# Kernel tuning notes

Measured on AMD Instinct MI355X. Metric: run time of the kernel, lower is better.

Reference implementation:

```python
import jax, jax.numpy as jnp
import numpy as np

H = 8        # attention heads
G = 8        # groupnorm groups
EPS = 1e-5

def mish(x):
    return x * jnp.tanh(jnp.logaddexp(x, 0.0))

def conv1d(x, w, b, pad):
    # x: [B,C,L], w: [O,I,K]
    y = jax.lax.conv_general_dilated(x, w, (1,), [(pad, pad)],
                                     dimension_numbers=('NCH', 'OIH', 'NCH'))
    return y + b[None, :, None]

def gn_per_step(x, gamma, beta):
    # torch code reshapes [B,C,L] -> [(B L), C] and applies GroupNorm(G, C):
    # normalize each (b, l) position over channel groups.
    B, C, L = x.shape
    xg = x.reshape(B, G, C // G, L)
    mean = xg.mean(axis=2, keepdims=True)
    var = xg.var(axis=2, keepdims=True)
    xg = (xg - mean) * jax.lax.rsqrt(var + EPS)
    return xg.reshape(B, C, L) * gamma[None, :, None] + beta[None, :, None]

def layernorm(x, g, b):
    mean = x.mean(axis=-1, keepdims=True)
    var = x.var(axis=-1, keepdims=True)
    return (x - mean) * jax.lax.rsqrt(var + EPS) * g + b


def setup_inputs() -> dict:
    key = jax.random.key(0)
    ks = jax.random.split(key, 16)
    B, Cin, Cout, L, N, CD, TD = 64, 256, 512, 512, 77, 768, 512
    w = lambda k, shape, s=0.02: (jax.random.normal(k, shape, jnp.float32) * s)
    return {
        'x': jax.random.normal(ks[0], (B, Cin, L), jnp.float32),
        't': jax.random.normal(ks[1], (B, TD), jnp.float32),
        'cond': jax.random.normal(ks[2], (B, N, CD), jnp.float32),
        'conv0_w': w(ks[3], (Cout, Cin, 5)), 'conv0_b': jnp.zeros((Cout,), jnp.float32),
        'gn0_g': jnp.ones((Cout,), jnp.float32), 'gn0_b': jnp.zeros((Cout,), jnp.float32),
        'tm_w': w(ks[4], (2 * Cout, TD)), 'tm_b': jnp.zeros((2 * Cout,), jnp.float32),
        'conv1_w': w(ks[5], (Cout, Cout, 5)), 'conv1_b': jnp.zeros((Cout,), jnp.float32),
        'gn1_g': jnp.ones((Cout,), jnp.float32), 'gn1_b': jnp.zeros((Cout,), jnp.float32),
        'res_w': w(ks[6], (Cout, Cin, 1)), 'res_b': jnp.zeros((Cout,), jnp.float32),
        'ln_x_g': jnp.ones((Cout,), jnp.float32), 'ln_x_b': jnp.zeros((Cout,), jnp.float32),
        'ln_c_g': jnp.ones((CD,), jnp.float32), 'ln_c_b': jnp.zeros((CD,), jnp.float32),
        'q_w': w(ks[7], (Cout, Cout)), 'q_b': jnp.zeros((Cout,), jnp.float32),
        'k_w': w(ks[8], (Cout, CD)), 'k_b': jnp.zeros((Cout,), jnp.float32),
        'v_w': w(ks[9], (Cout, CD)), 'v_b': jnp.zeros((Cout,), jnp.float32),
        'cond_indices': jnp.arange(B, dtype=jnp.int64 if jax.config.jax_enable_x64 else jnp.int32),
    }


def _forward(x, t, cond,
             conv0_w, conv0_b, gn0_g, gn0_b, tm_w, tm_b,
             conv1_w, conv1_b, gn1_g, gn1_b, res_w, res_b,
             ln_x_g, ln_x_b, ln_c_g, ln_c_b,
             q_w, q_b, k_w, k_b, v_w, v_b, cond_indices):
    Cout = conv0_w.shape[0]
    # ---- ResidualTemporalBlock (adagn=True) ----
    ss = jnp.einsum('bi,oi->bo', mish(t), tm_w) + tm_b        # [B, 2*Cout]
    scale = ss[:, :Cout, None]                                 # chunk dim=1
    shift = ss[:, Cout:, None]
    h = conv1d(x, conv0_w, conv0_b, pad=2)                     # [B,Cout,L]
    h = gn_per_step(h, gn0_g, gn0_b)
    h = mish(h * (1.0 + scale) + shift)                        # ada_shift_scale + Mish
    h = conv1d(h, conv1_w, conv1_b, pad=2)
    h = mish(gn_per_step(h, gn1_g, gn1_b))
    out = h + conv1d(x, res_w, res_b, pad=0)                   # residual 1x1 conv
    # ---- ResidualCrossAttentionLayer (LinearCrossAttention) ----
    xs = out[cond_indices]                                     # [Bc,Cout,L]
    xi = xs.transpose(0, 2, 1)                                 # [Bc,L,Cout]
    cs = cond[cond_indices]                                    # [Bc,N,CD]
    Bc, T, D = xi.shape
    Nn = cs.shape[1]
    Dh = D // H
    q = jnp.einsum('btl,dl->btd', layernorm(xi, ln_x_g, ln_x_b), q_w) + q_b
    cn = layernorm(cs, ln_c_g, ln_c_b)
    k = jnp.einsum('bnl,dl->bnd', cn, k_w) + k_b
    v = jnp.einsum('bnl,dl->bnd', cn, v_w) + v_b
    q = jax.nn.softmax(q.reshape(Bc, T, H, Dh), axis=-1)       # softmax over head dim
    k = jax.nn.softmax(k.reshape(Bc, Nn, H, Dh), axis=1)       # softmax over tokens
    v = v.reshape(Bc, Nn, H, Dh)
    attn = jnp.einsum('bnhd,bnhl->bhdl', k, v)                 # [Bc,H,Dh,Dh] kernel
    y = jnp.einsum('bthd,bhdl->bthl', q, attn).reshape(Bc, T, D)
    return out.at[cond_indices].add(y.transpose(0, 2, 1))


def reference(x, t, cond,
              conv0_w, conv0_b, gn0_g, gn0_b, tm_w, tm_b,
              conv1_w, conv1_b, gn1_g, gn1_b, res_w, res_b,
              ln_x_g, ln_x_b, ln_c_g, ln_c_b,
              q_w, q_b, k_w, k_b, v_w, v_b, cond_indices):
    return _forward(x, t, cond, conv0_w, conv0_b, gn0_g, gn0_b, tm_w, tm_b,
                    conv1_w, conv1_b, gn1_g, gn1_b, res_w, res_b,
                    ln_x_g, ln_x_b, ln_c_g, ln_c_b,
                    q_w, q_b, k_w, k_b, v_w, v_b, cond_indices)
```

## Files before the change

### kernel.cpp

```cpp
#include <hip/hip_runtime.h>
#include <math.h>

#define EPS 1e-5f

typedef __attribute__((ext_vector_type(8))) short short8;
typedef __attribute__((ext_vector_type(4))) float floatx4;

typedef __attribute__((address_space(1))) const void* gas1_t;
typedef __attribute__((address_space(3))) void* las3_t;

__device__ __forceinline__ void glls16(const void* g, void* l) {
    __builtin_amdgcn_global_load_lds((gas1_t)g, (las3_t)l, 16, 0, 0);
}

__device__ __forceinline__ float mishf(float x) {
    float sp = fmaxf(x, 0.0f) + log1pf(expf(-fabsf(x)));
    return x * tanhf(sp);
}
__device__ __forceinline__ unsigned short f2bf(float f) {
    unsigned int u = __float_as_uint(f);
    unsigned int r = (u + 0x7fffu + ((u >> 16) & 1u)) >> 16;
    return (unsigned short)r;
}
__device__ __forceinline__ float bf2f(unsigned short s) {
    return __uint_as_float(((unsigned int)s) << 16);
}
__device__ __forceinline__ unsigned int pk2(unsigned short a, unsigned short b) {
    return (unsigned int)a | ((unsigned int)b << 16);
}

__global__ __launch_bounds__(256) void mish_k(const float* __restrict__ t,
                                              float* __restrict__ mt, int n) {
    int i = blockIdx.x * 256 + threadIdx.x;
    if (i < n) mt[i] = mishf(t[i]);
}

__global__ __launch_bounds__(256) void pack_w(const float* __restrict__ w,
        unsigned short* __restrict__ wp, int CI, int KS, int n) {
    int o = blockIdx.x * 256 + threadIdx.x;
    if (o >= n) return;
    int ci = o % CI;
    int co = (o / CI) & 511;
    int kk = o / (CI * 512);
    wp[o] = f2bf(w[((size_t)co * CI + ci) * KS + kk]);
}

__global__ __launch_bounds__(256) void cvt_bf16(const float* __restrict__ src,
        unsigned short* __restrict__ dst, int n4) {
    int i = blockIdx.x * 256 + threadIdx.x;
    if (i >= n4) return;
    float4 f = *(const float4*)&src[(size_t)i * 4];
    *(uint2*)&dst[(size_t)i * 4] =
        make_uint2(pk2(f2bf(f.x), f2bf(f.y)), pk2(f2bf(f.z), f2bf(f.w)));
}

__global__ __launch_bounds__(256) void xpose_cvt(const float* __restrict__ x,
        unsigned short* __restrict__ xT) {
    __shared__ float tile[64][68];
    const int tid = threadIdx.x;
    const int l0 = blockIdx.x * 64, c0 = blockIdx.y * 64, b = blockIdx.z;
    for (int idx = tid; idx < 64 * 16; idx += 256) {
        int cr = idx >> 4, lc = (idx & 15) * 4;
        float4 f = *(const float4*)&x[((size_t)b * 256 + c0 + cr) * 512 + l0 + lc];
        tile[cr][lc] = f.x; tile[cr][lc + 1] = f.y;
        tile[cr][lc + 2] = f.z; tile[cr][lc + 3] = f.w;
    }
    __syncthreads();
    for (int idx = tid; idx < 64 * 16; idx += 256) {
        int lr = idx >> 4, cc = (idx & 15) * 4;
        *(uint2*)&xT[((size_t)b * 512 + l0 + lr) * 256 + c0 + cc] =
            make_uint2(pk2(f2bf(tile[cc][lr]), f2bf(tile[cc + 1][lr])),
                       pk2(f2bf(tile[cc + 2][lr]), f2bf(tile[cc + 3][lr])));
    }
}

template<int KD>
__global__ __launch_bounds__(256) void gemm_nt(const float* __restrict__ A,
        const float* __restrict__ W, const float* __restrict__ bias,
        float* __restrict__ C, int M, int N) {
    constexpr int ST = 20;
    __shared__ __align__(16) float As[64 * ST];
    __shared__ __align__(16) float Ws[64 * ST];
    const int tid = threadIdx.x;
    const int r0 = blockIdx.x * 64, c0 = blockIdx.y * 64;
    const int tx = tid & 15, ty = tid >> 4;
    const int lrow = tid >> 2, lk = (tid & 3) * 4;
    float acc[4][4];
#pragma unroll
    for (int i = 0; i < 4; ++i)
#pragma unroll
        for (int j = 0; j < 4; ++j) acc[i][j] = 0.f;
    for (int k0 = 0; k0 < KD; k0 += 16) {
        __syncthreads();
        *(float4*)&As[lrow * ST + lk] =
            *(const float4*)&A[(size_t)(r0 + lrow) * KD + k0 + lk];
        *(float4*)&Ws[lrow * ST + lk] =
            *(const float4*)&W[(size_t)(c0 + lrow) * KD + k0 + lk];
        __syncthreads();
#pragma unroll
        for (int kk = 0; kk < 16; kk += 4) {
            float4 av[4], wv[4];
#pragma unroll
            for (int i = 0; i < 4; ++i)
                av[i] = *(const float4*)&As[(ty + 16 * i) * ST + kk];
#pragma unroll
            for (int j = 0; j < 4; ++j)
                wv[j] = *(const float4*)&Ws[(tx + 16 * j) * ST + kk];
#pragma unroll
            for (int i = 0; i < 4; ++i)
#pragma unroll
                for (int j = 0; j < 4; ++j) {
                    acc[i][j] = fmaf(av[i].x, wv[j].x, acc[i][j]);
                    acc[i][j] = fmaf(av[i].y, wv[j].y, acc[i][j]);
                    acc[i][j] = fmaf(av[i].z, wv[j].z, acc[i][j]);
                    acc[i][j] = fmaf(av[i].w, wv[j].w, acc[i][j]);
                }
        }
    }
#pragma unroll
    for (int j = 0; j < 4; ++j) {
        int c = c0 + tx + 16 * j;
        float bv = bias[c];
#pragma unroll
        for (int i = 0; i < 4; ++i)
            C[(size_t)(r0 + ty + 16 * i) * N + c] = acc[i][j] + bv;
    }
}

template<int CI, bool FILM>
__global__ __launch_bounds__(256) void conv5_mfma(
        const unsigned short* __restrict__ xb,
        const unsigned short* __restrict__ wp,
        const float* __restrict__ bias,
        const float* __restrict__ gam, const float* __restrict__ bet,
        const float* __restrict__ ss,
        unsigned short* __restrict__ outT) {
    __shared__ __align__(16) unsigned short xs[260 * 32];
    __shared__ __align__(16) unsigned short wsm[5 * 64 * 32];
    __shared__ float sgam[64], sbet[64], sbias[64], sscale[64], sshift[64];

    const int tid = threadIdx.x;
    const int l0 = blockIdx.x * 256;
    const int co0 = blockIdx.y * 64;
    const int b = blockIdx.z;
    const int lane = tid & 63;
    const int wv = tid >> 6;
    const int lq = lane & 15, qd = lane >> 4;
    const int wn = wv * 64;

    if (tid < 64) {
        int co = co0 + tid;
        sbias[tid] = bias[co];
        sgam[tid] = gam[co];
        sbet[tid] = bet[co];
        if (FILM) {
            sscale[tid] = ss[(size_t)b * 1024 + co];
            sshift[tid] = ss[(size_t)b * 1024 + 512 + co];
        }
    }

    floatx4 acc[4][4];
#pragma unroll
    for (int i = 0; i < 4; ++i)
#pragma unroll
        for (int j = 0; j < 4; ++j) acc[i][j] = (floatx4){0.f, 0.f, 0.f, 0.f};

    for (int ci0 = 0; ci0 < CI; ci0 += 32) {
        __syncthreads();
        if (tid < 128) {
            int rh = tid >> 5;
            int lr = (rh < 2) ? rh : (256 + rh);
            int ci_l = tid & 31;
            int gl = l0 - 2 + lr;
            unsigned short v = 0;
            if (gl >= 0 && gl < 512)
                v = xb[((size_t)b * 512 + gl) * CI + ci0 + ci_l];
            int pos = (ci_l >> 3) ^ ((lr >> 1) & 3);
            xs[lr * 32 + pos * 8 + (ci_l & 7)] = v;
        }
        {
            const unsigned short* gb = &xb[((size_t)b * 512 + l0) * CI + ci0];
#pragma unroll
            for (int it = 0; it < 4; ++it) {
                int task = it * 256 + wv * 64 + lane;
                int ri = task >> 2, pos = task & 3;
                int seg = pos ^ (((ri + 2) >> 1) & 3);
                glls16(gb + (size_t)ri * CI + seg * 8,
                       (void*)(xs + 64 + (it * 256 + wv * 64) * 8));
            }
        }
        {
#pragma unroll
            for (int it = 0; it < 5; ++it) {
                int task = it * 256 + wv * 64 + lane;
                int kk = task >> 8;
                int r = task & 255;
                int co_l = r >> 2, pos = r & 3;
                int seg = pos ^ ((co_l >> 1) & 3);
                glls16(&wp[((size_t)(kk * 512 + co0 + co_l)) * CI + ci0 + seg * 8],
                       (void*)(wsm + (it * 256 + wv * 64) * 8));
            }
        }
        __syncthreads();
#pragma unroll
        for (int kk = 0; kk < 5; ++kk) {
            short8 bvf[4];
#pragma unroll
            for (int j = 0; j < 4; ++j) {
                int row = wn + j * 16 + lq + kk;
                int pos = qd ^ ((row >> 1) & 3);
                bvf[j] = *(const short8*)&xs[row * 32 + pos * 8];
            }
#pragma unroll
            for (int i = 0; i < 4; ++i) {
                int crow = i * 16 + lq;
                int pos = qd ^ ((crow >> 1) & 3);
                short8 av = *(const short8*)&wsm[kk * 2048 + crow * 32 + pos * 8];
#pragma unroll
                for (int j = 0; j < 4; ++j)
                    acc[i][j] = __builtin_amdgcn_mfma_f32_16x16x32_bf16(
                        av, bvf[j], acc[i][j], 0, 0, 0);
            }
        }
    }
    float m_[4], rs_[4];
#pragma unroll
    for (int j = 0; j < 4; ++j) {
        float s1 = 0.f, s2 = 0.f;
#pragma unroll
        for (int i = 0; i < 4; ++i) {
            float4 bv4 = *(const float4*)&sbias[i * 16 + qd * 4];
            float ba[4] = {bv4.x, bv4.y, bv4.z, bv4.w};
#pragma unroll
            for (int r = 0; r < 4; ++r) {
                float v = acc[i][j][r] + ba[r];
                acc[i][j][r] = v;
                s1 += v; s2 += v * v;
            }
        }
        s1 += __shfl_xor(s1, 16, 64); s2 += __shfl_xor(s2, 16, 64);
        s1 += __shfl_xor(s1, 32, 64); s2 += __shfl_xor(s2, 32, 64);
        float mean = s1 * (1.f / 64.f);
        float var = s2 * (1.f / 64.f) - mean * mean;
        m_[j] = mean; rs_[j] = rsqrtf(var + EPS);
    }
#pragma unroll
    for (int j = 0; j < 4; ++j) {
        int l = l0 + wn + j * 16 + lq;
        size_t rowbase = ((size_t)b * 512 + l) * 512 + co0;
#pragma unroll
        for (int i = 0; i < 4; ++i) {
            float4 g4 = *(const float4*)&sgam[i * 16 + qd * 4];
            float4 b4 = *(const float4*)&sbet[i * 16 + qd * 4];
            float ga[4] = {g4.x, g4.y, g4.z, g4.w};
            float be[4] = {b4.x, b4.y, b4.z, b4.w};
            float sa[4] = {0, 0, 0, 0}, sh[4] = {0, 0, 0, 0};
            if (FILM) {
                float4 s4 = *(const float4*)&sscale[i * 16 + qd * 4];
                float4 h4 = *(const float4*)&sshift[i * 16 + qd * 4];
                sa[0] = s4.x; sa[1] = s4.y; sa[2] = s4.z; sa[3] = s4.w;
                sh[0] = h4.x; sh[1] = h4.y; sh[2] = h4.z; sh[3] = h4.w;
            }
            unsigned short o[4];
#pragma unroll
            for (int r = 0; r < 4; ++r) {
                float v = (acc[i][j][r] - m_[j]) * rs_[j] * ga[r] + be[r];
                if (FILM) v = v * (1.f + sa[r]) + sh[r];
                o[r] = f2bf(mishf(v));
            }
            *(uint2*)&outT[rowbase + i * 16 + qd * 4] =
                make_uint2(pk2(o[0], o[1]), pk2(o[2], o[3]));
        }
    }
}

template<int KD, int EPI>
__global__ __launch_bounds__(256) void gemm1_mfma(
        const unsigned short* __restrict__ A,
        const unsigned short* __restrict__ W,
        const float* __restrict__ bias,
        const unsigned short* __restrict__ addT,
        float* __restrict__ outF,
        unsigned short* __restrict__ outB,
        int Mreal) {
    __shared__ __align__(16) unsigned short xs[256 * 32];
    __shared__ __align__(16) unsigned short wsm[64 * 32];
    __shared__ float sbias[64];
    const int tid = threadIdx.x;
    const int m0 = blockIdx.x * 256;
    const int n0 = blockIdx.y * 64;
    const int lane = tid & 63;
    const int wv = tid >> 6;
    const int lq = lane & 15, qd = lane >> 4;
    const int wn = wv * 64;
    if (tid < 64) sbias[tid] = bias[n0 + tid];

    floatx4 acc[4][4];
#pragma unroll
    for (int i = 0; i < 4; ++i)
#pragma unroll
        for (int j = 0; j < 4; ++j) acc[i][j] = (floatx4){0.f, 0.f, 0.f, 0.f};

    for (int ci0 = 0; ci0 < KD; ci0 += 32) {
        __syncthreads();
#pragma unroll
        for (int it = 0; it < 4; ++it) {
            int task = it * 256 + wv * 64 + lane;
            int ri = task >> 2, pos = task & 3;
            int seg = pos ^ ((ri >> 1) & 3);
            glls16(&A[((size_t)(m0 + ri)) * KD + ci0 + seg * 8],
                   (void*)(xs + (it * 256 + wv * 64) * 8));
        }
        {
            int task = wv * 64 + lane;
            int co_l = task >> 2, pos = task & 3;
            int seg = pos ^ ((co_l >> 1) & 3);
            glls16(&W[((size_t)(n0 + co_l)) * KD + ci0 + seg * 8],
                   (void*)(wsm + (wv * 64) * 8));
        }
        __syncthreads();
        short8 bvf[4];
#pragma unroll
        for (int j = 0; j < 4; ++j) {
            int row = wn + j * 16 + lq;
            int pos = qd ^ ((row >> 1) & 3);
            bvf[j] = *(const short8*)&xs[row * 32 + pos * 8];
        }
#pragma unroll
        for (int i = 0; i < 4; ++i) {
            int crow = i * 16 + lq;
            int pos = qd ^ ((crow >> 1) & 3);
            short8 av = *(const short8*)&wsm[crow * 32 + pos * 8];
#pragma unroll
            for (int j = 0; j < 4; ++j)
                acc[i][j] = __builtin_amdgcn_mfma_f32_16x16x32_bf16(
                    av, bvf[j], acc[i][j], 0, 0, 0);
        }
    }
#pragma unroll
    for (int i = 0; i < 4; ++i) {
        float4 bv4 = *(const float4*)&sbias[i * 16 + qd * 4];
        float ba[4] = {bv4.x, bv4.y, bv4.z, bv4.w};
#pragma unroll
        for (int j = 0; j < 4; ++j)
#pragma unroll
            for (int r = 0; r < 4; ++r) acc[i][j][r] += ba[r];
    }
    if (EPI == 0) {
#pragma unroll
        for (int j = 0; j < 4; ++j) {
            int m = m0 + wn + j * 16 + lq;
#pragma unroll
            for (int i = 0; i < 4; ++i) {
                int n = n0 + i * 16 + qd * 4;
                uint2 hv = *(const uint2*)&addT[(size_t)m * 512 + n];
                float vr[4];
                vr[0] = acc[i][j][0] + bf2f((unsigned short)(hv.x & 0xffff));
                vr[1] = acc[i][j][1] + bf2f((unsigned short)(hv.x >> 16));
                vr[2] = acc[i][j][2] + bf2f((unsigned short)(hv.y & 0xffff));
                vr[3] = acc[i][j][3] + bf2f((unsigned short)(hv.y >> 16));
                *(uint2*)&outB[(size_t)m * 512 + n] =
                    make_uint2(pk2(f2bf(vr[0]), f2bf(vr[1])),
                               pk2(f2bf(vr[2]), f2bf(vr[3])));
            }
        }
    } else if (EPI == 1) {
#pragma unroll
        for (int j = 0; j < 4; ++j) {
            float mx = -3.4e38f;
#pragma unroll
            for (int i = 0; i < 4; ++i)
#pragma unroll
                for (int r = 0; r < 4; ++r) mx = fmaxf(mx, acc[i][j][r]);
            mx = fmaxf(mx, __shfl_xor(mx, 16, 64));
            mx = fmaxf(mx, __shfl_xor(mx, 32, 64));
            float s = 0.f;
#pragma unroll
            for (int i = 0; i < 4; ++i)
#pragma unroll
                for (int r = 0; r < 4; ++r) {
                    float e = expf(acc[i][j][r] - mx);
                    acc[i][j][r] = e; s += e;
                }
            s += __shfl_xor(s, 16, 64);
            s += __shfl_xor(s, 32, 64);
            float inv = 1.f / s;
            int m = m0 + wn + j * 16 + lq;
#pragma unroll
            for (int i = 0; i < 4; ++i) {
                *(uint2*)&outB[(size_t)m * 512 + n0 + i * 16 + qd * 4] =
                    make_uint2(pk2(f2bf(acc[i][j][0] * inv), f2bf(acc[i][j][1] * inv)),
                               pk2(f2bf(acc[i][j][2] * inv), f2bf(acc[i][j][3] * inv)));
            }
        }
    } else {
#pragma unroll
        for (int j = 0; j < 4; ++j) {
            int m = m0 + wn + j * 16 + lq;
            if (m < Mreal) {
#pragma unroll
                for (int i = 0; i < 4; ++i) {
                    float4 o = {acc[i][j][0], acc[i][j][1], acc[i][j][2], acc[i][j][3]};
                    *(float4*)&outF[(size_t)m * 512 + n0 + i * 16 + qd * 4] = o;
                }
            }
        }
    }
}

__global__ __launch_bounds__(256) void lnrow(const unsigned short* __restrict__ src,
        const float* __restrict__ g, const float* __restrict__ be,
        const int* __restrict__ cidx, unsigned short* __restrict__ dst) {
    const int tid = threadIdx.x;
    const int lane = tid & 63, wv = tid >> 6;
    const int row0 = blockIdx.x * 32 + wv * 8;
    for (int rr = 0; rr < 8; ++rr) {
        int m = row0 + rr;
        int b = m >> 9, t = m & 511;
        int ib = cidx[b];
        const unsigned short* sp = &src[((size_t)ib * 512 + t) * 512 + lane * 8];
        short8 u = *(const short8*)sp;
        float v[8];
        float s1 = 0.f, s2 = 0.f;
#pragma unroll
        for (int k = 0; k < 8; ++k) {
            v[k] = bf2f(((const unsigned short*)&u)[k]);
            s1 += v[k]; s2 += v[k] * v[k];
        }
#pragma unroll
        for (int o = 32; o > 0; o >>= 1) {
            s1 += __shfl_xor(s1, o, 64);
            s2 += __shfl_xor(s2, o, 64);
        }
        float mean = s1 * (1.f / 512.f);
        float var = s2 * (1.f / 512.f) - mean * mean;
        float rs = rsqrtf(var + EPS);
        float4 g0 = *(const float4*)&g[lane * 8];
        float4 g1 = *(const float4*)&g[lane * 8 + 4];
        float4 b0 = *(const float4*)&be[lane * 8];
        float4 b1 = *(const float4*)&be[lane * 8 + 4];
        float ga[8] = {g0.x, g0.y, g0.z, g0.w, g1.x, g1.y, g1.z, g1.w};
        float ba[8] = {b0.x, b0.y, b0.z, b0.w, b1.x, b1.y, b1.z, b1.w};
        unsigned short o8[8];
#pragma unroll
        for (int k = 0; k < 8; ++k)
            o8[k] = f2bf((v[k] - mean) * rs * ga[k] + ba[k]);
        *(uint4*)&dst[(size_t)m * 512 + lane * 8] =
            make_uint4(pk2(o8[0], o8[1]), pk2(o8[2], o8[3]),
                       pk2(o8[4], o8[5]), pk2(o8[6], o8[7]));
    }
}

__global__ __launch_bounds__(256) void lnc_k(const float* __restrict__ cond,
        const float* __restrict__ g, const float* __restrict__ be,
        const int* __restrict__ cidx, unsigned short* __restrict__ cn) {
    const int tid = threadIdx.x;
    const int bn = blockIdx.x;
    const int b = bn / 77, n = bn - b * 77;
    const int ib = cidx[b];
    const float* src = cond + ((size_t)ib * 77 + n) * 768;
    float v[3];
    float s = 0.f, s2 = 0.f;
#pragma unroll
    for (int i = 0; i < 3; ++i) {
        v[i] = src[tid + i * 256];
        s += v[i]; s2 += v[i] * v[i];
    }
#pragma unroll
    for (int o = 32; o > 0; o >>= 1) {
        s += __shfl_xor(s, o, 64);
        s2 += __shfl_xor(s2, o, 64);
    }
    __shared__ float r1[4], r2[4], mv[2];
    if ((tid & 63) == 0) { r1[tid >> 6] = s; r2[tid >> 6] = s2; }
    __syncthreads();
    if (tid == 0) {
        float ts = r1[0] + r1[1] + r1[2] + r1[3];
        float ts2 = r2[0] + r2[1] + r2[2] + r2[3];
        float m = ts * (1.f / 768.f);
        float var = ts2 * (1.f / 768.f) - m * m;
        mv[0] = m; mv[1] = rsqrtf(var + EPS);
    }
    __syncthreads();
    float m = mv[0], rs = mv[1];
    unsigned short* dst = cn + ((size_t)b * 77 + n) * 768;
#pragma unroll
    for (int i = 0; i < 3; ++i) {
        int c = tid + i * 256;
        dst[c] = f2bf((v[i] - m) * rs * g[c] + be[c]);
    }
}

__global__ __launch_bounds__(256) void ksm_k(float* __restrict__ k) {
    int gid = blockIdx.x * 256 + threadIdx.x;
    int b = gid >> 9, d = gid & 511;
    float* p = k + (size_t)b * 77 * 512 + d;
    float mx = -3.4e38f;
    for (int n = 0; n < 77; ++n) mx = fmaxf(mx, p[(size_t)n * 512]);
    float s = 0.f;
    for (int n = 0; n < 77; ++n) s += expf(p[(size_t)n * 512] - mx);
    float inv = 1.f / s;
    for (int n = 0; n < 77; ++n)
        p[(size_t)n * 512] = expf(p[(size_t)n * 512] - mx) * inv;
}

__global__ __launch_bounds__(256) void attn_k(const float* __restrict__ k,
        const float* __restrict__ v, unsigned short* __restrict__ attnT) {
    constexpr int NS = 68;
    __shared__ __align__(16) float ks[77 * NS];
    __shared__ __align__(16) float vs[77 * NS];
    const int tid = threadIdx.x;
    const int b = blockIdx.x >> 3, h = blockIdx.x & 7;
    for (int idx = tid; idx < 77 * 16; idx += 256) {
        int n = idx >> 4, dq = (idx & 15) * 4;
        *(float4*)&ks[n * NS + dq] =
            *(const float4*)&k[((size_t)b * 77 + n) * 512 + h * 64 + dq];
        *(float4*)&vs[n * NS + dq] =
            *(const float4*)&v[((size_t)b * 77 + n) * 512 + h * 64 + dq];
    }
    __syncthreads();
    const int e = tid & 63, dq = tid >> 6;
    float acc[16];
#pragma unroll
    for (int u = 0; u < 16; ++u) acc[u] = 0.f;
    for (int n = 0; n < 77; ++n) {
        float vv = vs[n * NS + e];
#pragma unroll
        for (int u4 = 0; u4 < 4; ++u4) {
            float4 kk = *(const float4*)&ks[n * NS + dq * 16 + u4 * 4];
            acc[u4 * 4 + 0] = fmaf(kk.x, vv, acc[u4 * 4 + 0]);
            acc[u4 * 4 + 1] = fmaf(kk.y, vv, acc[u4 * 4 + 1]);
            acc[u4 * 4 + 2] = fmaf(kk.z, vv, acc[u4 * 4 + 2]);
            acc[u4 * 4 + 3] = fmaf(kk.w, vv, acc[u4 * 4 + 3]);
        }
    }
    unsigned short ob[16];
#pragma unroll
    for (int u = 0; u < 16; ++u) ob[u] = f2bf(acc[u]);
    size_t base = (((size_t)b * 8 + h) * 64 + e) * 64 + dq * 16;
    *(uint4*)&attnT[base] = make_uint4(pk2(ob[0], ob[1]), pk2(ob[2], ob[3]),
                                       pk2(ob[4], ob[5]), pk2(ob[6], ob[7]));
    *(uint4*)&attnT[base + 8] = make_uint4(pk2(ob[8], ob[9]), pk2(ob[10], ob[11]),
                                           pk2(ob[12], ob[13]), pk2(ob[14], ob[15]));
}

__global__ __launch_bounds__(256) void yattn_final(
        const unsigned short* __restrict__ q,
        const unsigned short* __restrict__ at,
        const unsigned short* __restrict__ resT,
        const int* __restrict__ cidx, float* __restrict__ out) {
    const int tid = threadIdx.x;
    const int lane = tid & 63, wv = tid >> 6;
    const int lq = lane & 15, qd = lane >> 4;
    const int t0 = blockIdx.x * 256 + wv * 64;
    const int h = blockIdx.y, b = blockIdx.z;
    const int ib = cidx[b];
    floatx4 acc[4][4];
#pragma unroll
    for (int i = 0; i < 4; ++i)
#pragma unroll
        for (int j = 0; j < 4; ++j) acc[i][j] = (floatx4){0.f, 0.f, 0.f, 0.f};
#pragma unroll
    for (int ks = 0; ks < 2; ++ks) {
        short8 av[4], bv[4];
#pragma unroll
        for (int i = 0; i < 4; ++i)
            av[i] = *(const short8*)
                &q[((size_t)(b * 512 + t0 + i * 16 + lq)) * 512 + h * 64 + ks * 32 + qd * 8];
#pragma unroll
        for (int j = 0; j < 4; ++j)
            bv[j] = *(const short8*)
                &at[(((size_t)(b * 8 + h)) * 64 + j * 16 + lq) * 64 + ks * 32 + qd * 8];
#pragma unroll
        for (int i = 0; i < 4; ++i)
#pragma unroll
            for (int j = 0; j < 4; ++j)
                acc[i][j] = __builtin_amdgcn_mfma_f32_16x16x32_bf16(
                    av[i], bv[j], acc[i][j], 0, 0, 0);
    }
#pragma unroll
    for (int j = 0; j < 4; ++j) {
        int c = h * 64 + j * 16 + lq;
#pragma unroll
        for (int i = 0; i < 4; ++i) {
            int tb = t0 + i * 16 + qd * 4;
            float4 o;
            float vr[4];
#pragma unroll
            for (int r = 0; r < 4; ++r)
                vr[r] = acc[i][j][r] +
                        bf2f(resT[((size_t)(ib * 512 + tb + r)) * 512 + c]);
            o.x = vr[0]; o.y = vr[1]; o.z = vr[2]; o.w = vr[3];
            *(float4*)&out[((size_t)ib * 512 + c) * 512 + tb] = o;
        }
    }
}

extern "C" void kernel_launch(void* const* d_in, const int* in_sizes, int n_in,
                              void* d_out, int out_size, void* d_ws, size_t ws_size,
                              hipStream_t stream) {
    (void)in_sizes; (void)n_in; (void)out_size; (void)ws_size;
    const float* x       = (const float*)d_in[0];
    const float* t       = (const float*)d_in[1];
    const float* cond    = (const float*)d_in[2];
    const float* conv0_w = (const float*)d_in[3];
    const float* conv0_b = (const float*)d_in[4];
    const float* gn0_g   = (const float*)d_in[5];
    const float* gn0_b   = (const float*)d_in[6];
    const float* tm_w    = (const float*)d_in[7];
    const float* tm_b    = (const float*)d_in[8];
    const float* conv1_w = (const float*)d_in[9];
    const float* conv1_b = (const float*)d_in[10];
    const float* gn1_g   = (const float*)d_in[11];
    const float* gn1_b   = (const float*)d_in[12];
    const float* res_w   = (const float*)d_in[13];
    const float* res_b   = (const float*)d_in[14];
    const float* ln_x_g  = (const float*)d_in[15];
    const float* ln_x_b  = (const float*)d_in[16];
    const float* ln_c_g  = (const float*)d_in[17];
    const float* ln_c_b  = (const float*)d_in[18];
    const float* q_w     = (const float*)d_in[19];
    const float* q_b     = (const float*)d_in[20];
    const float* k_w     = (const float*)d_in[21];
    const float* k_b     = (const float*)d_in[22];
    const float* v_w     = (const float*)d_in[23];
    const float* v_b     = (const float*)d_in[24];
    const int*   cidx    = (const int*)d_in[25];
    float* out = (float*)d_out;

    char* WS = (char*)d_ws;
    unsigned short* xT    = (unsigned short*)(WS + 0);
    unsigned short* cnb   = (unsigned short*)(WS + 0);
    unsigned short* attnT = (unsigned short*)(WS + 8388608);
    unsigned short* h0T   = (unsigned short*)(WS + 16777216);
    unsigned short* xlnT  = (unsigned short*)(WS + 16777216);
    float*          kb    = (float*)(WS + 16777216);
    float*          vb    = (float*)(WS + 26869760);
    unsigned short* h1T   = (unsigned short*)(WS + 50331648);
    unsigned short* qbf   = (unsigned short*)(WS + 50331648);
    unsigned short* outTb = (unsigned short*)(WS + 83886080);
    unsigned short* wp0   = (unsigned short*)(WS + 83886080);
    unsigned short* wp1   = (unsigned short*)(WS + 86507520);
    unsigned short* wr    = (unsigned short*)(WS + 117440512);
    unsigned short* wq    = (unsigned short*)(WS + 117702656);
    unsigned short* wk    = (unsigned short*)(WS + 118226944);
    unsigned short* wvv   = (unsigned short*)(WS + 119013376);
    float*          ssb   = (float*)(WS + 119799808);
    float*          mt    = (float*)(WS + 120061952);

    pack_w<<<dim3((512*256*5)/256), dim3(256), 0, stream>>>(conv0_w, wp0, 256, 5, 512*256*5);
    pack_w<<<dim3((512*512*5)/256), dim3(256), 0, stream>>>(conv1_w, wp1, 512, 5, 512*512*5);
    cvt_bf16<<<dim3(128),  dim3(256), 0, stream>>>(res_w, wr, 32768);
    cvt_bf16<<<dim3(256),  dim3(256), 0, stream>>>(q_w,   wq, 65536);
    cvt_bf16<<<dim3(384),  dim3(256), 0, stream>>>(k_w,   wk, 98304);
    cvt_bf16<<<dim3(384),  dim3(256), 0, stream>>>(v_w,   wvv, 98304);
    xpose_cvt<<<dim3(8, 4, 64), dim3(256), 0, stream>>>(x, xT);
    mish_k<<<dim3(128), dim3(256), 0, stream>>>(t, mt, 32768);
    gemm_nt<512><<<dim3(1, 16), dim3(256), 0, stream>>>(mt, tm_w, tm_b, ssb, 64, 1024);
    conv5_mfma<256, true><<<dim3(2, 8, 64), dim3(256), 0, stream>>>(
        xT, wp0, conv0_b, gn0_g, gn0_b, ssb, h0T);
    conv5_mfma<512, false><<<dim3(2, 8, 64), dim3(256), 0, stream>>>(
        h0T, wp1, conv1_b, gn1_g, gn1_b, (const float*)nullptr, h1T);
    gemm1_mfma<256, 0><<<dim3(128, 8), dim3(256), 0, stream>>>(
        xT, wr, res_b, h1T, (float*)nullptr, outTb, 32768);
    lnrow<<<dim3(1024), dim3(256), 0, stream>>>(outTb, ln_x_g, ln_x_b, cidx, xlnT);
    gemm1_mfma<512, 1><<<dim3(128, 8), dim3(256), 0, stream>>>(
        xlnT, wq, q_b, (const unsigned short*)nullptr, (float*)nullptr, qbf, 32768);
    lnc_k<<<dim3(4928), dim3(256), 0, stream>>>(cond, ln_c_g, ln_c_b, cidx, cnb);
    gemm1_mfma<768, 2><<<dim3(20, 8), dim3(256), 0, stream>>>(
        cnb, wk, k_b, (const unsigned short*)nullptr, kb, (unsigned short*)nullptr, 4928);
    gemm1_mfma<768, 2><<<dim3(20, 8), dim3(256), 0, stream>>>(
        cnb, wvv, v_b, (const unsigned short*)nullptr, vb, (unsigned short*)nullptr, 4928);
    ksm_k<<<dim3(128), dim3(256), 0, stream>>>(kb);
    attn_k<<<dim3(512), dim3(256), 0, stream>>>(kb, vb, attnT);
    yattn_final<<<dim3(2, 8, 64), dim3(256), 0, stream>>>(qbf, attnT, outTb, cidx, out);
}
```

Baseline: 651.5 us.

## Double-buffer conv and GEMM LDS staging, pad activations, fuse setup and key softmax

Conv5 and 1x1 GEMM kernels now use two LDS buffers so global-to-LDS loads for the next K-chunk overlap MFMA work on the current one, with one barrier per iteration. Activations are stored with two zero rows of padding per batch, which removes the scalar halo-load path in the conv. The six weight-packing, mish and padding-zeroing launches are merged into one setup kernel, and the key softmax is folded into the attention kernel, removing a separate pass. Doubling LDS per block may lower occupancy, and the workspace layout was reshuffled.

```diff
diff --git a/kernel.cpp b/kernel.cpp
--- a/kernel.cpp
+++ b/kernel.cpp
@@ -29,29 +29,61 @@
     return (unsigned int)a | ((unsigned int)b << 16);
 }
 
-__global__ __launch_bounds__(256) void mish_k(const float* __restrict__ t,
-                                              float* __restrict__ mt, int n) {
-    int i = blockIdx.x * 256 + threadIdx.x;
-    if (i < n) mt[i] = mishf(t[i]);
-}
-
-__global__ __launch_bounds__(256) void pack_w(const float* __restrict__ w,
-        unsigned short* __restrict__ wp, int CI, int KS, int n) {
-    int o = blockIdx.x * 256 + threadIdx.x;
-    if (o >= n) return;
-    int ci = o % CI;
-    int co = (o / CI) & 511;
-    int kk = o / (CI * 512);
-    wp[o] = f2bf(w[((size_t)co * CI + ci) * KS + kk]);
-}
-
-__global__ __launch_bounds__(256) void cvt_bf16(const float* __restrict__ src,
-        unsigned short* __restrict__ dst, int n4) {
-    int i = blockIdx.x * 256 + threadIdx.x;
-    if (i >= n4) return;
-    float4 f = *(const float4*)&src[(size_t)i * 4];
-    *(uint2*)&dst[(size_t)i * 4] =
-        make_uint2(pk2(f2bf(f.x), f2bf(f.y)), pk2(f2bf(f.z), f2bf(f.w)));
+__global__ __launch_bounds__(256) void setup_k(
+        const float* __restrict__ conv0_w, const float* __restrict__ conv1_w,
+        const float* __restrict__ res_w, const float* __restrict__ q_w,
+        const float* __restrict__ k_w, const float* __restrict__ v_w,
+        const float* __restrict__ t,
+        unsigned short* __restrict__ wp0, unsigned short* __restrict__ wp1,
+        unsigned short* __restrict__ wr, unsigned short* __restrict__ wq,
+        unsigned short* __restrict__ wk, unsigned short* __restrict__ wvv,
+        float* __restrict__ mt,
+        unsigned short* __restrict__ xTp, unsigned short* __restrict__ h0Tp) {
+    const int blk = blockIdx.x, tid = threadIdx.x;
+    if (blk < 2560) {
+        int o = blk * 256 + tid;
+        int ci = o & 255, co = (o >> 8) & 511, kk = o >> 17;
+        wp0[o] = f2bf(conv0_w[((size_t)co * 256 + ci) * 5 + kk]);
+    } else if (blk < 7680) {
+        int o = (blk - 2560) * 256 + tid;
+        int ci = o & 511, co = (o >> 9) & 511, kk = o >> 18;
+        wp1[o] = f2bf(conv1_w[((size_t)co * 512 + ci) * 5 + kk]);
+    } else if (blk < 7808) {
+        int i = (blk - 7680) * 256 + tid;
+        float4 f = *(const float4*)&res_w[(size_t)i * 4];
+        *(uint2*)&wr[(size_t)i * 4] =
+            make_uint2(pk2(f2bf(f.x), f2bf(f.y)), pk2(f2bf(f.z), f2bf(f.w)));
+    } else if (blk < 8064) {
+        int i = (blk - 7808) * 256 + tid;
+        float4 f = *(const float4*)&q_w[(size_t)i * 4];
+        *(uint2*)&wq[(size_t)i * 4] =
+            make_uint2(pk2(f2bf(f.x), f2bf(f.y)), pk2(f2bf(f.z), f2bf(f.w)));
+    } else if (blk < 8448) {
+        int i = (blk - 8064) * 256 + tid;
+        float4 f = *(const float4*)&k_w[(size_t)i * 4];
+        *(uint2*)&wk[(size_t)i * 4] =
+            make_uint2(pk2(f2bf(f.x), f2bf(f.y)), pk2(f2bf(f.z), f2bf(f.w)));
+    } else if (blk < 8832) {
+        int i = (blk - 8448) * 256 + tid;
+        float4 f = *(const float4*)&v_w[(size_t)i * 4];
+        *(uint2*)&wvv[(size_t)i * 4] =
+            make_uint2(pk2(f2bf(f.x), f2bf(f.y)), pk2(f2bf(f.z), f2bf(f.w)));
+    } else if (blk < 8960) {
+        int i = (blk - 8832) * 256 + tid;
+        mt[i] = mishf(t[i]);
+    } else if (blk < 8992) {
+        int idx = (blk - 8960) * 256 + tid;
+        int u = idx * 8;
+        int c = u & 255, r4 = (u >> 8) & 3, b = u >> 10;
+        int row = (r4 < 2) ? r4 : (512 + r4);
+        *(uint4*)&xTp[((size_t)b * 516 + row) * 256 + c] = make_uint4(0, 0, 0, 0);
+    } else {
+        int idx = (blk - 8992) * 256 + tid;
+        int u = idx * 8;
+        int c = u & 511, r4 = (u >> 9) & 3, b = u >> 11;
+        int row = (r4 < 2) ? r4 : (512 + r4);
+        *(uint4*)&h0Tp[((size_t)b * 516 + row) * 512 + c] = make_uint4(0, 0, 0, 0);
+    }
 }
 
 __global__ __launch_bounds__(256) void xpose_cvt(const float* __restrict__ x,
@@ -68,7 +100,7 @@
     __syncthreads();
     for (int idx = tid; idx < 64 * 16; idx += 256) {
         int lr = idx >> 4, cc = (idx & 15) * 4;
-        *(uint2*)&xT[((size_t)b * 512 + l0 + lr) * 256 + c0 + cc] =
+        *(uint2*)&xT[((size_t)b * 516 + 2 + l0 + lr) * 256 + c0 + cc] =
             make_uint2(pk2(f2bf(tile[cc][lr]), f2bf(tile[cc + 1][lr])),
                        pk2(f2bf(tile[cc + 2][lr]), f2bf(tile[cc + 3][lr])));
     }
@@ -127,7 +159,7 @@
     }
 }
 
-template<int CI, bool FILM>
+template<int CI, bool FILM, bool OPAD>
 __global__ __launch_bounds__(256) void conv5_mfma(
         const unsigned short* __restrict__ xb,
         const unsigned short* __restrict__ wp,
@@ -135,8 +167,9 @@
         const float* __restrict__ gam, const float* __restrict__ bet,
         const float* __restrict__ ss,
         unsigned short* __restrict__ outT) {
-    __shared__ __align__(16) unsigned short xs[260 * 32];
-    __shared__ __align__(16) unsigned short wsm[5 * 64 * 32];
+    constexpr int NC = CI / 32;
+    __shared__ __align__(16) unsigned short xs[2][260 * 32];
+    __shared__ __align__(16) unsigned short wsm[2][5 * 64 * 32];
     __shared__ float sgam[64], sbet[64], sbias[64], sscale[64], sshift[64];
 
     const int tid = threadIdx.x;
@@ -159,49 +192,46 @@
         }
     }
 
+    const unsigned short* gxb = xb + ((size_t)b * 516 + l0) * CI;
+    const unsigned short* gwb = wp + (size_t)co0 * CI;
+
+    auto stage = [&](int c, int buf) {
+        const unsigned short* gx = gxb + c * 32;
+        unsigned short* xd = (unsigned short*)xs[buf];
+#pragma unroll
+        for (int it = 0; it < 5; ++it) {
+            int task = it * 256 + tid;
+            if (task < 1040) {
+                int ri = task >> 2, pos = task & 3;
+                int seg = pos ^ ((ri >> 1) & 3);
+                glls16(gx + (size_t)ri * CI + seg * 8, xd + (it * 256 + wn) * 8);
+            }
+        }
+        const unsigned short* gw = gwb + c * 32;
+        unsigned short* wd = (unsigned short*)wsm[buf];
+#pragma unroll
+        for (int it = 0; it < 5; ++it) {
+            int task = it * 256 + tid;
+            int kk = task >> 8, r = task & 255;
+            int col = r >> 2, pos = r & 3;
+            int seg = pos ^ ((col >> 1) & 3);
+            glls16(gw + ((size_t)kk * 512 + col) * CI + seg * 8,
+                   wd + (it * 256 + wn) * 8);
+        }
+    };
+
     floatx4 acc[4][4];
 #pragma unroll
     for (int i = 0; i < 4; ++i)
 #pragma unroll
         for (int j = 0; j < 4; ++j) acc[i][j] = (floatx4){0.f, 0.f, 0.f, 0.f};
 
-    for (int ci0 = 0; ci0 < CI; ci0 += 32) {
-        __syncthreads();
-        if (tid < 128) {
-            int rh = tid >> 5;
-            int lr = (rh < 2) ? rh : (256 + rh);
-            int ci_l = tid & 31;
-            int gl = l0 - 2 + lr;
-            unsigned short v = 0;
-            if (gl >= 0 && gl < 512)
-                v = xb[((size_t)b * 512 + gl) * CI + ci0 + ci_l];
-            int pos = (ci_l >> 3) ^ ((lr >> 1) & 3);
-            xs[lr * 32 + pos * 8 + (ci_l & 7)] = v;
-        }
-        {
-            const unsigned short* gb = &xb[((size_t)b * 512 + l0) * CI + ci0];
-#pragma unroll
-            for (int it = 0; it < 4; ++it) {
-                int task = it * 256 + wv * 64 + lane;
-                int ri = task >> 2, pos = task & 3;
-                int seg = pos ^ (((ri + 2) >> 1) & 3);
-                glls16(gb + (size_t)ri * CI + seg * 8,
-                       (void*)(xs + 64 + (it * 256 + wv * 64) * 8));
-            }
-        }
-        {
-#pragma unroll
-            for (int it = 0; it < 5; ++it) {
-                int task = it * 256 + wv * 64 + lane;
-                int kk = task >> 8;
-                int r = task & 255;
-                int co_l = r >> 2, pos = r & 3;
-                int seg = pos ^ ((co_l >> 1) & 3);
-                glls16(&wp[((size_t)(kk * 512 + co0 + co_l)) * CI + ci0 + seg * 8],
-                       (void*)(wsm + (it * 256 + wv * 64) * 8));
-            }
-        }
-        __syncthreads();
+    stage(0, 0);
+    __syncthreads();
+    for (int c = 0; c < NC; ++c) {
+        if (c + 1 < NC) stage(c + 1, (c + 1) & 1);
+        const unsigned short* xr = (const unsigned short*)xs[c & 1];
+        const unsigned short* wr_ = (const unsigned short*)wsm[c & 1];
 #pragma unroll
         for (int kk = 0; kk < 5; ++kk) {
             short8 bvf[4];
@@ -209,19 +239,20 @@
             for (int j = 0; j < 4; ++j) {
                 int row = wn + j * 16 + lq + kk;
                 int pos = qd ^ ((row >> 1) & 3);
-                bvf[j] = *(const short8*)&xs[row * 32 + pos * 8];
+                bvf[j] = *(const short8*)&xr[row * 32 + pos * 8];
             }
 #pragma unroll
             for (int i = 0; i < 4; ++i) {
                 int crow = i * 16 + lq;
                 int pos = qd ^ ((crow >> 1) & 3);
-                short8 av = *(const short8*)&wsm[kk * 2048 + crow * 32 + pos * 8];
+                short8 av = *(const short8*)&wr_[kk * 2048 + crow * 32 + pos * 8];
 #pragma unroll
                 for (int j = 0; j < 4; ++j)
                     acc[i][j] = __builtin_amdgcn_mfma_f32_16x16x32_bf16(
                         av, bvf[j], acc[i][j], 0, 0, 0);
             }
         }
+        __syncthreads();
     }
     float m_[4], rs_[4];
 #pragma unroll
@@ -247,7 +278,8 @@
 #pragma unroll
     for (int j = 0; j < 4; ++j) {
         int l = l0 + wn + j * 16 + lq;
-        size_t rowbase = ((size_t)b * 512 + l) * 512 + co0;
+        size_t rowbase = OPAD ? (((size_t)b * 516 + 2 + l) * 512 + co0)
+                              : (((size_t)b * 512 + l) * 512 + co0);
 #pragma unroll
         for (int i = 0; i < 4; ++i) {
             float4 g4 = *(const float4*)&sgam[i * 16 + qd * 4];
@@ -274,7 +306,7 @@
     }
 }
 
-template<int KD, int EPI>
+template<int KD, int EPI, bool PADA>
 __global__ __launch_bounds__(256) void gemm1_mfma(
         const unsigned short* __restrict__ A,
         const unsigned short* __restrict__ W,
@@ -283,8 +315,9 @@
         float* __restrict__ outF,
         unsigned short* __restrict__ outB,
         int Mreal) {
-    __shared__ __align__(16) unsigned short xs[256 * 32];
-    __shared__ __align__(16) unsigned short wsm[64 * 32];
+    constexpr int NC = KD / 32;
+    __shared__ __align__(16) unsigned short xs[2][256 * 32];
+    __shared__ __align__(16) unsigned short wsm[2][64 * 32];
     __shared__ float sbias[64];
     const int tid = threadIdx.x;
     const int m0 = blockIdx.x * 256;
@@ -295,47 +328,60 @@
     const int wn = wv * 64;
     if (tid < 64) sbias[tid] = bias[n0 + tid];
 
-    floatx4 acc[4][4];
-#pragma unroll
-    for (int i = 0; i < 4; ++i)
-#pragma unroll
-        for (int j = 0; j < 4; ++j) acc[i][j] = (floatx4){0.f, 0.f, 0.f, 0.f};
-
-    for (int ci0 = 0; ci0 < KD; ci0 += 32) {
-        __syncthreads();
+    const size_t arow0 = PADA ? ((size_t)(m0 >> 9) * 516 + 2 + (m0 & 511))
+                              : (size_t)m0;
+    const unsigned short* gA = A + arow0 * KD;
+    const unsigned short* gW = W + (size_t)n0 * KD;
+
+    auto stage = [&](int c, int buf) {
+        const unsigned short* gx = gA + c * 32;
+        unsigned short* xd = (unsigned short*)xs[buf];
 #pragma unroll
         for (int it = 0; it < 4; ++it) {
-            int task = it * 256 + wv * 64 + lane;
+            int task = it * 256 + tid;
             int ri = task >> 2, pos = task & 3;
             int seg = pos ^ ((ri >> 1) & 3);
-            glls16(&A[((size_t)(m0 + ri)) * KD + ci0 + seg * 8],
-                   (void*)(xs + (it * 256 + wv * 64) * 8));
-        }
+            glls16(gx + (size_t)ri * KD + seg * 8, xd + (it * 256 + wn) * 8);
+        }
+        const unsigned short* gw = gW + c * 32;
+        unsigned short* wd = (unsigned short*)wsm[buf];
         {
-            int task = wv * 64 + lane;
-            int co_l = task >> 2, pos = task & 3;
-            int seg = pos ^ ((co_l >> 1) & 3);
-            glls16(&W[((size_t)(n0 + co_l)) * KD + ci0 + seg * 8],
-                   (void*)(wsm + (wv * 64) * 8));
-        }
-        __syncthreads();
+            int col = tid >> 2, pos = tid & 3;
+            int seg = pos ^ ((col >> 1) & 3);
+            glls16(gw + (size_t)col * KD + seg * 8, wd + wn * 8);
+        }
+    };
+
+    floatx4 acc[4][4];
+#pragma unroll
+    for (int i = 0; i < 4; ++i)
+#pragma unroll
+        for (int j = 0; j < 4; ++j) acc[i][j] = (floatx4){0.f, 0.f, 0.f, 0.f};
+
+    stage(0, 0);
+    __syncthreads();
+    for (int c = 0; c < NC; ++c) {
+        if (c + 1 < NC) stage(c + 1, (c + 1) & 1);
+        const unsigned short* xr = (const unsigned short*)xs[c & 1];
+        const unsigned short* wr_ = (const unsigned short*)wsm[c & 1];
         short8 bvf[4];
 #pragma unroll
         for (int j = 0; j < 4; ++j) {
             int row = wn + j * 16 + lq;
             int pos = qd ^ ((row >> 1) & 3);
-            bvf[j] = *(const short8*)&xs[row * 32 + pos * 8];
+            bvf[j] = *(const short8*)&xr[row * 32 + pos * 8];
         }
 #pragma unroll
         for (int i = 0; i < 4; ++i) {
             int crow = i * 16 + lq;
             int pos = qd ^ ((crow >> 1) & 3);
-            short8 av = *(const short8*)&wsm[crow * 32 + pos * 8];
+            short8 av = *(const short8*)&wr_[crow * 32 + pos * 8];
 #pragma unroll
             for (int j = 0; j < 4; ++j)
                 acc[i][j] = __builtin_amdgcn_mfma_f32_16x16x32_bf16(
                     av, bvf[j], acc[i][j], 0, 0, 0);
         }
+        __syncthreads();
     }
 #pragma unroll
     for (int i = 0; i < 4; ++i) {
@@ -491,32 +537,39 @@
     }
 }
 
-__global__ __launch_bounds__(256) void ksm_k(float* __restrict__ k) {
-    int gid = blockIdx.x * 256 + threadIdx.x;
-    int b = gid >> 9, d = gid & 511;
-    float* p = k + (size_t)b * 77 * 512 + d;
-    float mx = -3.4e38f;
-    for (int n = 0; n < 77; ++n) mx = fmaxf(mx, p[(size_t)n * 512]);
-    float s = 0.f;
-    for (int n = 0; n < 77; ++n) s += expf(p[(size_t)n * 512] - mx);
-    float inv = 1.f / s;
-    for (int n = 0; n < 77; ++n)
-        p[(size_t)n * 512] = expf(p[(size_t)n * 512] - mx) * inv;
-}
-
 __global__ __launch_bounds__(256) void attn_k(const float* __restrict__ k,
         const float* __restrict__ v, unsigned short* __restrict__ attnT) {
     constexpr int NS = 68;
     __shared__ __align__(16) float ks[77 * NS];
     __shared__ __align__(16) float vs[77 * NS];
+    __shared__ float red[2][256];
     const int tid = threadIdx.x;
     const int b = blockIdx.x >> 3, h = blockIdx.x & 7;
     for (int idx = tid; idx < 77 * 16; idx += 256) {
-        int n = idx >> 4, dq = (idx & 15) * 4;
-        *(float4*)&ks[n * NS + dq] =
-            *(const float4*)&k[((size_t)b * 77 + n) * 512 + h * 64 + dq];
-        *(float4*)&vs[n * NS + dq] =
-            *(const float4*)&v[((size_t)b * 77 + n) * 512 + h * 64 + dq];
+        int n = idx >> 4, dq2 = (idx & 15) * 4;
+        *(float4*)&ks[n * NS + dq2] =
+            *(const float4*)&k[((size_t)b * 77 + n) * 512 + h * 64 + dq2];
+        *(float4*)&vs[n * NS + dq2] =
+            *(const float4*)&v[((size_t)b * 77 + n) * 512 + h * 64 + dq2];
+    }
+    __syncthreads();
+    {
+        const int d = tid & 63, grp = tid >> 6;
+        float mx = -3.4e38f;
+        for (int n = grp; n < 77; n += 4) mx = fmaxf(mx, ks[n * NS + d]);
+        red[0][grp * 64 + d] = mx;
+        __syncthreads();
+        mx = fmaxf(fmaxf(red[0][d], red[0][64 + d]),
+                   fmaxf(red[0][128 + d], red[0][192 + d]));
+        float s = 0.f;
+        for (int n = grp; n < 77; n += 4) {
+            float e = expf(ks[n * NS + d] - mx);
+            ks[n * NS + d] = e; s += e;
+        }
+        red[1][grp * 64 + d] = s;
+        __syncthreads();
+        float inv = 1.f / (red[1][d] + red[1][64 + d] + red[1][128 + d] + red[1][192 + d]);
+        for (int n = grp; n < 77; n += 4) ks[n * NS + d] *= inv;
     }
     __syncthreads();
     const int e = tid & 63, dq = tid >> 6;
@@ -584,13 +637,12 @@
 #pragma unroll
         for (int i = 0; i < 4; ++i) {
             int tb = t0 + i * 16 + qd * 4;
-            float4 o;
             float vr[4];
 #pragma unroll
             for (int r = 0; r < 4; ++r)
                 vr[r] = acc[i][j][r] +
                         bf2f(resT[((size_t)(ib * 512 + tb + r)) * 512 + c]);
-            o.x = vr[0]; o.y = vr[1]; o.z = vr[2]; o.w = vr[3];
+            float4 o = {vr[0], vr[1], vr[2], vr[3]};
             *(float4*)&out[((size_t)ib * 512 + c) * 512 + tb] = o;
         }
     }
@@ -629,49 +681,44 @@
     float* out = (float*)d_out;
 
     char* WS = (char*)d_ws;
-    unsigned short* xT    = (unsigned short*)(WS + 0);
+    unsigned short* xTp   = (unsigned short*)(WS + 0);
     unsigned short* cnb   = (unsigned short*)(WS + 0);
     unsigned short* attnT = (unsigned short*)(WS + 8388608);
-    unsigned short* h0T   = (unsigned short*)(WS + 16777216);
-    unsigned short* xlnT  = (unsigned short*)(WS + 16777216);
-    float*          kb    = (float*)(WS + 16777216);
-    float*          vb    = (float*)(WS + 26869760);
-    unsigned short* h1T   = (unsigned short*)(WS + 50331648);
-    unsigned short* qbf   = (unsigned short*)(WS + 50331648);
-    unsigned short* outTb = (unsigned short*)(WS + 83886080);
-    unsigned short* wp0   = (unsigned short*)(WS + 83886080);
-    unsigned short* wp1   = (unsigned short*)(WS + 86507520);
-    unsigned short* wr    = (unsigned short*)(WS + 117440512);
-    unsigned short* wq    = (unsigned short*)(WS + 117702656);
-    unsigned short* wk    = (unsigned short*)(WS + 118226944);
-    unsigned short* wvv   = (unsigned short*)(WS + 119013376);
-    float*          ssb   = (float*)(WS + 119799808);
-    float*          mt    = (float*)(WS + 120061952);
-
-    pack_w<<<dim3((512*256*5)/256), dim3(256), 0, stream>>>(conv0_w, wp0, 256, 5, 512*256*5);
-    pack_w<<<dim3((512*512*5)/256), dim3(256), 0, stream>>>(conv1_w, wp1, 512, 5, 512*512*5);
-    cvt_bf16<<<dim3(128),  dim3(256), 0, stream>>>(res_w, wr, 32768);
-    cvt_bf16<<<dim3(256),  dim3(256), 0, stream>>>(q_w,   wq, 65536);
-    cvt_bf16<<<dim3(384),  dim3(256), 0, stream>>>(k_w,   wk, 98304);
-    cvt_bf16<<<dim3(384),  dim3(256), 0, stream>>>(v_w,   wvv, 98304);
-    xpose_cvt<<<dim3(8, 4, 64), dim3(256), 0, stream>>>(x, xT);
-    mish_k<<<dim3(128), dim3(256), 0, stream>>>(t, mt, 32768);
+    unsigned short* h0Tp  = (unsigned short*)(WS + 16908288);
+    unsigned short* xlnT  = (unsigned short*)(WS + 16908288);
+    float*          kb    = (float*)(WS + 16908288);
+    float*          vb    = (float*)(WS + 27000832);
+    unsigned short* h1T   = (unsigned short*)(WS + 50724864);
+    unsigned short* qbf   = (unsigned short*)(WS + 50724864);
+    unsigned short* outTb = (unsigned short*)(WS + 84279296);
+    unsigned short* wp0   = (unsigned short*)(WS + 117833728);
+    unsigned short* wp1   = (unsigned short*)(WS + 119144448);
+    unsigned short* wr    = (unsigned short*)(WS + 121765888);
+    unsigned short* wq    = (unsigned short*)(WS + 122028032);
+    unsigned short* wk    = (unsigned short*)(WS + 122552320);
+    unsigned short* wvv   = (unsigned short*)(WS + 123338752);
+    float*          ssb   = (float*)(WS + 124125184);
+    float*          mt    = (float*)(WS + 124387328);
+
+    setup_k<<<dim3(9056), dim3(256), 0, stream>>>(
+        conv0_w, conv1_w, res_w, q_w, k_w, v_w, t,
+        wp0, wp1, wr, wq, wk, wvv, mt, xTp, h0Tp);
+    xpose_cvt<<<dim3(8, 4, 64), dim3(256), 0, stream>>>(x, xTp);
     gemm_nt<512><<<dim3(1, 16), dim3(256), 0, stream>>>(mt, tm_w, tm_b, ssb, 64, 1024);
-    conv5_mfma<256, true><<<dim3(2, 8, 64), dim3(256), 0, stream>>>(
-        xT, wp0, conv0_b, gn0_g, gn0_b, ssb, h0T);
-    conv5_mfma<512, false><<<dim3(2, 8, 64), dim3(256), 0, stream>>>(
-        h0T, wp1, conv1_b, gn1_g, gn1_b, (const float*)nullptr, h1T);
-    gemm1_mfma<256, 0><<<dim3(128, 8), dim3(256), 0, stream>>>(
-        xT, wr, res_b, h1T, (float*)nullptr, outTb, 32768);
+    conv5_mfma<256, true, true><<<dim3(2, 8, 64), dim3(256), 0, stream>>>(
+        xTp, wp0, conv0_b, gn0_g, gn0_b, ssb, h0Tp);
+    conv5_mfma<512, false, false><<<dim3(2, 8, 64), dim3(256), 0, stream>>>(
+        h0Tp, wp1, conv1_b, gn1_g, gn1_b, (const float*)nullptr, h1T);
+    gemm1_mfma<256, 0, true><<<dim3(128, 8), dim3(256), 0, stream>>>(
+        xTp, wr, res_b, h1T, (float*)nullptr, outTb, 32768);
     lnrow<<<dim3(1024), dim3(256), 0, stream>>>(outTb, ln_x_g, ln_x_b, cidx, xlnT);
-    gemm1_mfma<512, 1><<<dim3(128, 8), dim3(256), 0, stream>>>(
+    gemm1_mfma<512, 1, false><<<dim3(128, 8), dim3(256), 0, stream>>>(
         xlnT, wq, q_b, (const unsigned short*)nullptr, (float*)nullptr, qbf, 32768);
     lnc_k<<<dim3(4928), dim3(256), 0, stream>>>(cond, ln_c_g, ln_c_b, cidx, cnb);
-    gemm1_mfma<768, 2><<<dim3(20, 8), dim3(256), 0, stream>>>(
+    gemm1_mfma<768, 2, false><<<dim3(20, 8), dim3(256), 0, stream>>>(
         cnb, wk, k_b, (const unsigned short*)nullptr, kb, (unsigned short*)nullptr, 4928);
-    gemm1_mfma<768, 2><<<dim3(20, 8), dim3(256), 0, stream>>>(
+    gemm1_mfma<768, 2, false><<<dim3(20, 8), dim3(256), 0, stream>>>(
         cnb, wvv, v_b, (const unsigned short*)nullptr, vb, (unsigned short*)nullptr, 4928);
-    ksm_k<<<dim3(128), dim3(256), 0, stream>>>(kb);
     attn_k<<<dim3(512), dim3(256), 0, stream>>>(kb, vb, attnT);
     yattn_final<<<dim3(2, 8, 64), dim3(256), 0, stream>>>(qbf, attnT, outTb, cidx, out);
 }
```

Result: faster. 612.5 us (-6.0%).
